# Kernel tuning notes

Hardware: AMD Instinct MI355X
Metric: run time of the kernel (lower is better)

## Reference

```python
import jax, jax.numpy as jnp
import numpy as np

N, R, D, K = 2048, 64, 64, 512  # batch, n_roles, filler_embed_dim, n_fillers
LAMBDA_VQ, LAMBDA_COMMIT, LAMBDA_ORTH = 1.0, 0.5, 0.0


def setup_inputs() -> dict:
    key = jax.random.key(0)
    k1, k2 = jax.random.split(key)
    soft_fillers = jax.random.normal(k1, (N, R, D), dtype=jnp.float32)
    weight = jax.random.normal(k2, (K, D), dtype=jnp.float32)  # codebook rows
    return {"soft_fillers": soft_fillers, "weight": weight}


def _nearest(x, w):
    # x: [M, D], w: [K, D] -> nearest codebook rows + indices
    d = (jnp.sum(x * x, axis=-1, keepdims=True)
         - 2.0 * (x @ w.T)
         + jnp.sum(w * w, axis=-1))          # [M, K]
    idx = jnp.argmin(d, axis=-1)              # [M]
    return w[idx], idx                        # gather: [M, D]


def reference(soft_fillers, weight):
    flat = soft_fillers.reshape(-1, D)        # [N*R, D]

    # Path 1: weight_sg=True -> weight detached, straight-through to input
    q_sg_flat, idx = _nearest(flat, jax.lax.stop_gradient(weight))
    q_sg_flat = flat + jax.lax.stop_gradient(q_sg_flat - flat)

    # Path 2: input detached -> gradient flows to weight via gather
    q_flat, _ = _nearest(jax.lax.stop_gradient(flat), weight)

    q_sg = q_sg_flat.reshape(N, R, D)
    q = q_flat.reshape(N, R, D)
    filler_idxs = idx.reshape(N, R)

    # vq loss: mean over (N, D) of L2-norm over roles of elementwise-squared diff
    t_vq = (q - jax.lax.stop_gradient(soft_fillers)) ** 2          # [N, R, D]
    vq_loss = jnp.mean(jnp.sqrt(jnp.sum(t_vq * t_vq, axis=1)))
    t_c = (jax.lax.stop_gradient(q) - soft_fillers) ** 2
    commit_loss = jnp.mean(jnp.sqrt(jnp.sum(t_c * t_c, axis=1)))

    # semi-orthogonality penalty on weight.t() (rows of codebook): ||W^T W - I||_F
    gram = weight.T @ weight                                        # [D, D]
    orth_penalty = jnp.linalg.norm(gram - jnp.eye(D, dtype=weight.dtype))

    total_loss = (LAMBDA_VQ * vq_loss + LAMBDA_COMMIT * commit_loss
                  + LAMBDA_ORTH * orth_penalty)

    filler_rank = jnp.linalg.matrix_rank(weight).astype(jnp.float32)

    return (total_loss, vq_loss, commit_loss, orth_penalty, filler_rank,
            q_sg, q, filler_idxs)
```

## Files before the change

### kernel.cpp

```cpp
#include <hip/hip_runtime.h>
#include <math.h>

#define N_ 2048
#define R_ 64
#define D_ 64
#define K_ 512
#define M_ (N_*R_)
#define TAU 0.012f
#define CHK 0.012f

#define WN_OFF   16
#define GRAM_OFF 1024
#define WBF_BYTE 32768
#define WS_NEED  163840

typedef __attribute__((ext_vector_type(8))) short s16x8;
typedef __attribute__((ext_vector_type(4))) float f32x4;

static __device__ __forceinline__ unsigned short f2bf(float f) {
    unsigned u = __float_as_uint(f);
    u += 0x7FFFu + ((u >> 16) & 1u);
    return (unsigned short)(u >> 16);
}
static __device__ __forceinline__ float bf2f(unsigned short h) {
    return __uint_as_float(((unsigned)h) << 16);
}

static __device__ __forceinline__ int xs_byte(int r, int q) {
    return r * 256 + (q >> 3) * 128 + (((q & 7) ^ (r & 7)) * 16);
}

static __device__ __forceinline__ void split8(const float* vv, s16x8& ph, s16x8& pl) {
#pragma unroll
    for (int j = 0; j < 8; ++j) {
        const unsigned short hb = f2bf(vv[j]);
        ph[j] = (short)hb;
        pl[j] = (short)f2bf(vv[j] - bf2f(hb));
    }
}

__global__ void k_pre(const float* __restrict__ w, float* __restrict__ ws, int pre) {
    const int b = blockIdx.x, t = threadIdx.x;
    if (b < 64) {
        __shared__ float red[4][64];
        const int i = b, j = t & 63, kg = t >> 6;
        float s = 0.f;
        for (int k = kg * 128; k < kg * 128 + 128; ++k)
            s = fmaf(w[k * 64 + i], w[k * 64 + j], s);
        red[kg][j] = s;
        __syncthreads();
        if (t < 64)
            ws[GRAM_OFF + i * 64 + t] = red[0][t] + red[1][t] + red[2][t] + red[3][t];
    } else if (b < 66) {
        const int code = (b - 64) * 256 + t;
        const float4* wr = (const float4*)(w + code * 64);
        float s = 0.f;
#pragma unroll
        for (int i = 0; i < 16; ++i) {
            float4 v = wr[i];
            s += v.x * v.x + v.y * v.y + v.z * v.z + v.w * v.w;
        }
        ws[WN_OFF + code] = s;
        if (b == 64 && t == 0) ws[0] = 0.f;
    } else {
        if (!pre) return;
        const int code = (b - 66) * 256 + t;
        char* whi = (char*)ws + WBF_BYTE;
        char* wlo = whi + 65536;
        const int c = code >> 6, rr = code & 63;
        const int nt = rr >> 4, lr = rr & 15;
        for (int kg = 0; kg < 8; ++kg) {
            float4 v0 = *(const float4*)(w + code * 64 + kg * 8);
            float4 v1 = *(const float4*)(w + code * 64 + kg * 8 + 4);
            const float vv[8] = {v0.x, v0.y, v0.z, v0.w, v1.x, v1.y, v1.z, v1.w};
            s16x8 ph, pl;
            split8(vv, ph, pl);
            const int s = kg >> 2, g = kg & 3, l = g * 16 + lr;
            const int off = (((c * 2 + s) * 4 + nt) << 10) + l * 16;
            *(s16x8*)(whi + off) = ph;
            *(s16x8*)(wlo + off) = pl;
        }
    }
}

template<bool PRE>
__global__ __launch_bounds__(256, 4) void k_argmin(
    const float* __restrict__ x, const float* __restrict__ w,
    float* __restrict__ ws, float* __restrict__ out)
{
    __shared__ __align__(16) float xs[8192];
    __shared__ __align__(16) float redw[2][4][64];
    __shared__ float fb1[128], fb2[128];
    __shared__ int   ridx[128];
    __shared__ int   ulist[128];
    __shared__ int   nunc;

    const int t = threadIdx.x;
    const int l = t & 63, wid = t >> 6;
    const int g = l >> 4, lr = l & 15;
    const long brow = (long)blockIdx.x * 128;
    const float* wn_g = ws + WN_OFF;
    const char* whi = (const char*)ws + WBF_BYTE;
    const char* wlo = whi + 65536;

    if (t == 0) nunc = 0;

#pragma unroll
    for (int ii = 0; ii < 8; ++ii) {
        const int gid = ii * 256 + t;
        const int r = gid >> 4, qq = gid & 15;
        const float4 v = *(const float4*)(x + (brow + r) * 64 + qq * 4);
        *(float4*)((char*)xs + xs_byte(r, qq)) = v;
    }
    __syncthreads();

    s16x8 ah[2][2], al[2][2];
#pragma unroll
    for (int mt = 0; mt < 2; ++mt) {
        const int row = wid * 32 + mt * 16 + lr;
#pragma unroll
        for (int s = 0; s < 2; ++s) {
            const int kg = s * 4 + g;
            const float4 v0 = *(const float4*)((const char*)xs + xs_byte(row, kg * 2));
            const float4 v1 = *(const float4*)((const char*)xs + xs_byte(row, kg * 2 + 1));
            const float vv[8] = {v0.x, v0.y, v0.z, v0.w, v1.x, v1.y, v1.z, v1.w};
            split8(vv, ah[mt][s], al[mt][s]);
        }
    }

    float b1[2][4], b2[2][4]; int i1[2][4];
#pragma unroll
    for (int mt = 0; mt < 2; ++mt)
#pragma unroll
        for (int j = 0; j < 4; ++j) { b1[mt][j] = 3.4e38f; b2[mt][j] = 3.4e38f; i1[mt][j] = 0; }

    for (int c = 0; c < 8; ++c) {
        f32x4 acc[2][4];
        const f32x4 z = {0.f, 0.f, 0.f, 0.f};
#pragma unroll
        for (int mt = 0; mt < 2; ++mt)
#pragma unroll
            for (int nt = 0; nt < 4; ++nt) acc[mt][nt] = z;

#pragma unroll
        for (int half = 0; half < 2; ++half) {
            s16x8 bh[2][2], bl[2][2];
#pragma unroll
            for (int s = 0; s < 2; ++s)
#pragma unroll
                for (int nth = 0; nth < 2; ++nth) {
                    const int nt = half * 2 + nth;
                    if constexpr (PRE) {
                        const int off = (((c * 2 + s) * 4 + nt) << 10) + l * 16;
                        bh[s][nth] = *(const s16x8*)(whi + off);
                        bl[s][nth] = *(const s16x8*)(wlo + off);
                    } else {
                        const int crow = c * 64 + nt * 16 + lr;
                        const float* src = w + (long)crow * 64 + (s * 4 + g) * 8;
                        const float4 v0 = *(const float4*)src;
                        const float4 v1 = *(const float4*)(src + 4);
                        const float vv[8] = {v0.x, v0.y, v0.z, v0.w, v1.x, v1.y, v1.z, v1.w};
                        split8(vv, bh[s][nth], bl[s][nth]);
                    }
                }
#pragma unroll
            for (int s = 0; s < 2; ++s)
#pragma unroll
                for (int nth = 0; nth < 2; ++nth) {
                    const int nt = half * 2 + nth;
#pragma unroll
                    for (int mt = 0; mt < 2; ++mt) {
                        acc[mt][nt] = __builtin_amdgcn_mfma_f32_16x16x32_bf16(ah[mt][s], bh[s][nth], acc[mt][nt], 0, 0, 0);
                        acc[mt][nt] = __builtin_amdgcn_mfma_f32_16x16x32_bf16(al[mt][s], bh[s][nth], acc[mt][nt], 0, 0, 0);
                        acc[mt][nt] = __builtin_amdgcn_mfma_f32_16x16x32_bf16(ah[mt][s], bl[s][nth], acc[mt][nt], 0, 0, 0);
                    }
                }
        }

#pragma unroll
        for (int nt = 0; nt < 4; ++nt) {
            const int code = c * 64 + nt * 16 + lr;
            const float wnv = wn_g[code];
#pragma unroll
            for (int mt = 0; mt < 2; ++mt)
#pragma unroll
                for (int j = 0; j < 4; ++j) {
                    const float sv = fmaf(-2.f, acc[mt][nt][j], wnv);
                    if (sv < b1[mt][j]) { b2[mt][j] = b1[mt][j]; b1[mt][j] = sv; i1[mt][j] = code; }
                    else if (sv < b2[mt][j]) b2[mt][j] = sv;
                }
        }
    }

#pragma unroll
    for (int m = 1; m < 16; m <<= 1) {
#pragma unroll
        for (int mt = 0; mt < 2; ++mt)
#pragma unroll
            for (int j = 0; j < 4; ++j) {
                const float ov1 = __shfl_xor(b1[mt][j], m, 64);
                const int   oi1 = __shfl_xor(i1[mt][j], m, 64);
                const float ov2 = __shfl_xor(b2[mt][j], m, 64);
                const float nb2 = fminf(fminf(b2[mt][j], ov2), fmaxf(b1[mt][j], ov1));
                if (ov1 < b1[mt][j] || (ov1 == b1[mt][j] && oi1 < i1[mt][j])) {
                    b1[mt][j] = ov1; i1[mt][j] = oi1;
                }
                b2[mt][j] = nb2;
            }
    }
    if (lr == 0) {
#pragma unroll
        for (int mt = 0; mt < 2; ++mt)
#pragma unroll
            for (int j = 0; j < 4; ++j) {
                const int ro = wid * 32 + mt * 16 + g * 4 + j;
                ridx[ro] = i1[mt][j];
                fb1[ro] = b1[mt][j];
                fb2[ro] = b2[mt][j];
            }
    }
    __syncthreads();

    {
        const int r = t >> 1, sub = t & 1;
        const int ci = ridx[r];
        const float* wrow = w + (long)ci * 64 + sub * 32;
        float dot = 0.f;
#pragma unroll
        for (int p = 0; p < 8; ++p) {
            const float4 xv = *(const float4*)((const char*)xs + xs_byte(r, sub * 8 + p));
            const float4 wv = *(const float4*)(wrow + p * 4);
            dot = fmaf(xv.x, wv.x, dot);
            dot = fmaf(xv.y, wv.y, dot);
            dot = fmaf(xv.z, wv.z, dot);
            dot = fmaf(xv.w, wv.w, dot);
        }
        dot += __shfl_xor(dot, 1, 64);
        if (sub == 0) {
            const float sex = fmaf(-2.f, dot, wn_g[ci]);
            const bool unc = ((fb2[r] - fb1[r]) < TAU) || (fabsf(sex - fb1[r]) > CHK);
            if (unc) { const int p = atomicAdd(&nunc, 1); ulist[p] = r; }
        }
    }
    __syncthreads();

    const int nu = nunc;
    if (nu > 0) {
        for (int e = wid; e < nu; e += 4) {
            const int r = ulist[e];
            float bv = 3.4e38f; int bi = 0;
            for (int cc = 0; cc < 8; ++cc) {
                const int code = cc * 64 + l;
                const float* wrow = w + (long)code * 64;
                float dot = 0.f;
#pragma unroll
                for (int p = 0; p < 16; ++p) {
                    const float4 xv = *(const float4*)((const char*)xs + xs_byte(r, p));
                    const float4 wv = *(const float4*)(wrow + p * 4);
                    dot = fmaf(xv.x, wv.x, dot);
                    dot = fmaf(xv.y, wv.y, dot);
                    dot = fmaf(xv.z, wv.z, dot);
                    dot = fmaf(xv.w, wv.w, dot);
                }
                const float sv = fmaf(-2.f, dot, wn_g[code]);
                if (sv < bv) { bv = sv; bi = code; }
            }
#pragma unroll
            for (int m = 1; m < 64; m <<= 1) {
                const float ov = __shfl_xor(bv, m, 64);
                const int   oi = __shfl_xor(bi, m, 64);
                if (ov < bv || (ov == bv && oi < bi)) { bv = ov; bi = oi; }
            }
            if (l == 0) ridx[r] = bi;
        }
    }
    __syncthreads();

    float* q_sg = out + 5;
    float* q    = out + 5 + (long)M_ * 64;
    float* fidx = out + 5 + 2L * M_ * 64;
    const int qq = t & 15, ry = t >> 4;
    float4 va = {0.f, 0.f, 0.f, 0.f}, vb = {0.f, 0.f, 0.f, 0.f};
#pragma unroll
    for (int ii = 0; ii < 8; ++ii) {
        const int r = ii * 16 + ry;
        const int ci = ridx[r];
        const float4 wv4 = *(const float4*)(w + (long)ci * 64 + qq * 4);
        const float4 xv4 = *(const float4*)((const char*)xs + xs_byte(r, qq));
        const long off = (brow + r) * 64 + qq * 4;
        *(float4*)(q_sg + off) = wv4;
        *(float4*)(q + off) = wv4;
        float4 p;
        p.x = (wv4.x - xv4.x) * (wv4.x - xv4.x);
        p.y = (wv4.y - xv4.y) * (wv4.y - xv4.y);
        p.z = (wv4.z - xv4.z) * (wv4.z - xv4.z);
        p.w = (wv4.w - xv4.w) * (wv4.w - xv4.w);
        float4 p2;
        p2.x = p.x * p.x; p2.y = p.y * p.y; p2.z = p.z * p.z; p2.w = p.w * p.w;
        if (ii < 4) {
            va.x += p2.x; va.y += p2.y; va.z += p2.z; va.w += p2.w;
        } else {
            vb.x += p2.x; vb.y += p2.y; vb.z += p2.z; vb.w += p2.w;
        }
    }
#pragma unroll
    for (int m = 16; m < 64; m <<= 1) {
        va.x += __shfl_xor(va.x, m, 64); va.y += __shfl_xor(va.y, m, 64);
        va.z += __shfl_xor(va.z, m, 64); va.w += __shfl_xor(va.w, m, 64);
        vb.x += __shfl_xor(vb.x, m, 64); vb.y += __shfl_xor(vb.y, m, 64);
        vb.z += __shfl_xor(vb.z, m, 64); vb.w += __shfl_xor(vb.w, m, 64);
    }
    if (l < 16) {
        *(float4*)&redw[0][wid][l * 4] = va;
        *(float4*)&redw[1][wid][l * 4] = vb;
    }
    if (t < 128) fidx[brow + t] = (float)ridx[t];
    __syncthreads();

    if (t < 128) {
        const int n = t >> 6, d = t & 63;
        const float s = redw[n][0][d] + redw[n][1][d] + redw[n][2][d] + redw[n][3][d];
        float v = sqrtf(s);
#pragma unroll
        for (int m = 1; m < 64; m <<= 1) v += __shfl_xor(v, m, 64);
        if (d == 0) atomicAdd(ws + 0, v);
    }
}

__global__ void k_final(const float* __restrict__ ws, float* __restrict__ out)
{
    __shared__ float g[64][65];
    __shared__ float osum[4];
    __shared__ float tol;
    const int t = threadIdx.x;
    float oacc = 0.f;
    for (int i = t; i < 4096; i += 256) {
        const int r = i >> 6, cl = i & 63;
        const float gv = ws[GRAM_OFF + i];
        g[r][cl] = gv;
        const float p = gv - (r == cl ? 1.f : 0.f);
        oacc = fmaf(p, p, oacc);
    }
#pragma unroll
    for (int m = 1; m < 64; m <<= 1) oacc += __shfl_xor(oacc, m, 64);
    if ((t & 63) == 0) osum[t >> 6] = oacc;
    __syncthreads();

    if (t == 0) {
        float maxd = 0.f;
        for (int i = 0; i < 64; ++i) maxd = fmaxf(maxd, fabsf(g[i][i]));
        tol = maxd * 1e-7f + 1e-30f;
    }
    __syncthreads();

    int rank = 0;
    const int j = t & 63, rq = t >> 6;
    for (int s = 0; s < 64; ++s) {
        const float p = g[s][s];
        const bool ok = fabsf(p) > tol;
        if (ok) {
            rank++;
            if (j > s) {
                const float rp = 1.f / p;
                const float gsj = g[s][j];
                for (int r = s + 1 + rq; r < 64; r += 4)
                    g[r][j] = fmaf(-(g[r][s] * rp), gsj, g[r][j]);
            }
        }
        __syncthreads();
    }

    if (t == 0) {
        const float vq = ws[0] / (float)(N_ * D_);
        const float orth = sqrtf(osum[0] + osum[1] + osum[2] + osum[3]);
        out[0] = 1.5f * vq;
        out[1] = vq;
        out[2] = vq;
        out[3] = orth;
        out[4] = (float)rank;
    }
}

extern "C" void kernel_launch(void* const* d_in, const int* in_sizes, int n_in,
                              void* d_out, int out_size, void* d_ws, size_t ws_size,
                              hipStream_t stream) {
    const float* x = (const float*)d_in[0];
    const float* w = (const float*)d_in[1];
    float* out = (float*)d_out;
    float* ws  = (float*)d_ws;
    const int pre = (ws_size >= (size_t)WS_NEED) ? 1 : 0;

    hipLaunchKernelGGL(k_pre, dim3(68), dim3(256), 0, stream, w, ws, pre);
    if (pre)
        hipLaunchKernelGGL((k_argmin<true>),  dim3(1024), dim3(256), 0, stream, x, w, ws, out);
    else
        hipLaunchKernelGGL((k_argmin<false>), dim3(1024), dim3(256), 0, stream, x, w, ws, out);
    hipLaunchKernelGGL(k_final, dim3(1), dim3(256), 0, stream, ws, out);
}
```

Measured before the change: 171.3 us.

## Software-pipeline codebook fragment loads, relax launch bounds, use nontemporal output stores

Restructures the argmin MFMA loop into a fully unrolled 16-step pipeline that loads the next half-chunk's codebook fragments into a double buffer while computing the current one, to hide global-load latency. Launch bounds drop from 4 to 2 blocks per SM, giving the compiler more registers for the extra buffers at the cost of occupancy. Output stores for q_sg, q and the index array become nontemporal to reduce cache pollution on the large streaming writes.

```diff
diff --git a/kernel.cpp b/kernel.cpp
--- a/kernel.cpp
+++ b/kernel.cpp
@@ -37,6 +37,11 @@
         ph[j] = (short)hb;
         pl[j] = (short)f2bf(vv[j] - bf2f(hb));
     }
+}
+
+static __device__ __forceinline__ void nt_store4(float* p, float x0, float x1, float x2, float x3) {
+    f32x4 v = {x0, x1, x2, x3};
+    __builtin_nontemporal_store(v, (f32x4*)p);
 }
 
 __global__ void k_pre(const float* __restrict__ w, float* __restrict__ ws, int pre) {
@@ -84,7 +89,7 @@
 }
 
 template<bool PRE>
-__global__ __launch_bounds__(256, 4) void k_argmin(
+__global__ __launch_bounds__(256, 2) void k_argmin(
     const float* __restrict__ x, const float* __restrict__ w,
     float* __restrict__ ws, float* __restrict__ out)
 {
@@ -134,62 +139,81 @@
 #pragma unroll
         for (int j = 0; j < 4; ++j) { b1[mt][j] = 3.4e38f; b2[mt][j] = 3.4e38f; i1[mt][j] = 0; }
 
-    for (int c = 0; c < 8; ++c) {
-        f32x4 acc[2][4];
-        const f32x4 z = {0.f, 0.f, 0.f, 0.f};
-#pragma unroll
-        for (int mt = 0; mt < 2; ++mt)
-#pragma unroll
-            for (int nt = 0; nt < 4; ++nt) acc[mt][nt] = z;
-
-#pragma unroll
-        for (int half = 0; half < 2; ++half) {
-            s16x8 bh[2][2], bl[2][2];
-#pragma unroll
-            for (int s = 0; s < 2; ++s)
-#pragma unroll
-                for (int nth = 0; nth < 2; ++nth) {
-                    const int nt = half * 2 + nth;
-                    if constexpr (PRE) {
-                        const int off = (((c * 2 + s) * 4 + nt) << 10) + l * 16;
-                        bh[s][nth] = *(const s16x8*)(whi + off);
-                        bl[s][nth] = *(const s16x8*)(wlo + off);
-                    } else {
-                        const int crow = c * 64 + nt * 16 + lr;
-                        const float* src = w + (long)crow * 64 + (s * 4 + g) * 8;
-                        const float4 v0 = *(const float4*)src;
-                        const float4 v1 = *(const float4*)(src + 4);
-                        const float vv[8] = {v0.x, v0.y, v0.z, v0.w, v1.x, v1.y, v1.z, v1.w};
-                        split8(vv, bh[s][nth], bl[s][nth]);
+    s16x8 pbh[2][4], pbl[2][4];
+    float4 pv0[2][4], pv1[2][4];
+    f32x4 acc[2][4];
+
+    auto issue = [&](int h, int par) {
+        const int c = h >> 1, half = h & 1;
+#pragma unroll
+        for (int s = 0; s < 2; ++s)
+#pragma unroll
+            for (int nth = 0; nth < 2; ++nth) {
+                const int nt = half * 2 + nth, idx = s * 2 + nth;
+                if constexpr (PRE) {
+                    const int off = (((c * 2 + s) * 4 + nt) << 10) + l * 16;
+                    pbh[par][idx] = *(const s16x8*)(whi + off);
+                    pbl[par][idx] = *(const s16x8*)(wlo + off);
+                } else {
+                    const int crow = c * 64 + nt * 16 + lr;
+                    const float* src = w + (long)crow * 64 + (s * 4 + g) * 8;
+                    pv0[par][idx] = *(const float4*)src;
+                    pv1[par][idx] = *(const float4*)(src + 4);
+                }
+            }
+    };
+
+    auto compute = [&](int h, int par) {
+        const int c = h >> 1, half = h & 1;
+        if (half == 0) {
+            const f32x4 z = {0.f, 0.f, 0.f, 0.f};
+#pragma unroll
+            for (int mt = 0; mt < 2; ++mt)
+#pragma unroll
+                for (int nt = 0; nt < 4; ++nt) acc[mt][nt] = z;
+        }
+#pragma unroll
+        for (int s = 0; s < 2; ++s)
+#pragma unroll
+            for (int nth = 0; nth < 2; ++nth) {
+                const int nt = half * 2 + nth, idx = s * 2 + nth;
+                s16x8 BH, BL;
+                if constexpr (PRE) {
+                    BH = pbh[par][idx]; BL = pbl[par][idx];
+                } else {
+                    const float4 v0 = pv0[par][idx], v1 = pv1[par][idx];
+                    const float vv[8] = {v0.x, v0.y, v0.z, v0.w, v1.x, v1.y, v1.z, v1.w};
+                    split8(vv, BH, BL);
+                }
+#pragma unroll
+                for (int mt = 0; mt < 2; ++mt) {
+                    acc[mt][nt] = __builtin_amdgcn_mfma_f32_16x16x32_bf16(ah[mt][s], BH, acc[mt][nt], 0, 0, 0);
+                    acc[mt][nt] = __builtin_amdgcn_mfma_f32_16x16x32_bf16(al[mt][s], BH, acc[mt][nt], 0, 0, 0);
+                    acc[mt][nt] = __builtin_amdgcn_mfma_f32_16x16x32_bf16(ah[mt][s], BL, acc[mt][nt], 0, 0, 0);
+                }
+            }
+        if (half == 1) {
+#pragma unroll
+            for (int nt = 0; nt < 4; ++nt) {
+                const int code = c * 64 + nt * 16 + lr;
+                const float wnv = wn_g[code];
+#pragma unroll
+                for (int mt = 0; mt < 2; ++mt)
+#pragma unroll
+                    for (int j = 0; j < 4; ++j) {
+                        const float sv = fmaf(-2.f, acc[mt][nt][j], wnv);
+                        if (sv < b1[mt][j]) { b2[mt][j] = b1[mt][j]; b1[mt][j] = sv; i1[mt][j] = code; }
+                        else if (sv < b2[mt][j]) b2[mt][j] = sv;
                     }
-                }
-#pragma unroll
-            for (int s = 0; s < 2; ++s)
-#pragma unroll
-                for (int nth = 0; nth < 2; ++nth) {
-                    const int nt = half * 2 + nth;
-#pragma unroll
-                    for (int mt = 0; mt < 2; ++mt) {
-                        acc[mt][nt] = __builtin_amdgcn_mfma_f32_16x16x32_bf16(ah[mt][s], bh[s][nth], acc[mt][nt], 0, 0, 0);
-                        acc[mt][nt] = __builtin_amdgcn_mfma_f32_16x16x32_bf16(al[mt][s], bh[s][nth], acc[mt][nt], 0, 0, 0);
-                        acc[mt][nt] = __builtin_amdgcn_mfma_f32_16x16x32_bf16(ah[mt][s], bl[s][nth], acc[mt][nt], 0, 0, 0);
-                    }
-                }
-        }
-
-#pragma unroll
-        for (int nt = 0; nt < 4; ++nt) {
-            const int code = c * 64 + nt * 16 + lr;
-            const float wnv = wn_g[code];
-#pragma unroll
-            for (int mt = 0; mt < 2; ++mt)
-#pragma unroll
-                for (int j = 0; j < 4; ++j) {
-                    const float sv = fmaf(-2.f, acc[mt][nt][j], wnv);
-                    if (sv < b1[mt][j]) { b2[mt][j] = b1[mt][j]; b1[mt][j] = sv; i1[mt][j] = code; }
-                    else if (sv < b2[mt][j]) b2[mt][j] = sv;
-                }
-        }
+            }
+        }
+    };
+
+    issue(0, 0);
+#pragma unroll
+    for (int h = 0; h < 16; ++h) {
+        if (h < 15) issue(h + 1, (h + 1) & 1);
+        compute(h, h & 1);
     }
 
 #pragma unroll
@@ -288,8 +312,8 @@
         const float4 wv4 = *(const float4*)(w + (long)ci * 64 + qq * 4);
         const float4 xv4 = *(const float4*)((const char*)xs + xs_byte(r, qq));
         const long off = (brow + r) * 64 + qq * 4;
-        *(float4*)(q_sg + off) = wv4;
-        *(float4*)(q + off) = wv4;
+        nt_store4(q_sg + off, wv4.x, wv4.y, wv4.z, wv4.w);
+        nt_store4(q + off,    wv4.x, wv4.y, wv4.z, wv4.w);
         float4 p;
         p.x = (wv4.x - xv4.x) * (wv4.x - xv4.x);
         p.y = (wv4.y - xv4.y) * (wv4.y - xv4.y);
@@ -314,7 +338,7 @@
         *(float4*)&redw[0][wid][l * 4] = va;
         *(float4*)&redw[1][wid][l * 4] = vb;
     }
-    if (t < 128) fidx[brow + t] = (float)ridx[t];
+    if (t < 128) __builtin_nontemporal_store((float)ridx[t], fidx + brow + t);
     __syncthreads();
 
     if (t < 128) {
```

After: 164.5 us. 4.0% less time.
